# Kernel tuning notes

Measured on AMD Instinct MI355X. Metric: run time of the kernel, lower is better.

Reference implementation:

```python
import jax, jax.numpy as jnp
import numpy as np

OUTCOMES = [8, 8, 8, 8, 8, 8]           # concept outcome counts (concepts_order)
N_TOTAL = int(np.prod(OUTCOMES))        # 262144 joint states
N_VALID = 8192                          # admissible states
B, D = 4096, 1024


def setup_inputs() -> dict:
    key = jax.random.key(0)
    k1, k2 = jax.random.split(key)
    embeddings = jax.random.normal(k1, (B, D), dtype=jnp.float32)
    W = jax.random.normal(k2, (N_VALID, D), dtype=jnp.float32) * 0.02
    b = jnp.zeros((N_VALID,), dtype=jnp.float32)
    # unique sorted admissible-state indices, like torch.argwhere(mask)
    rng = np.random.default_rng(0)
    valid_states = jnp.asarray(
        np.sort(rng.choice(N_TOTAL, size=N_VALID, replace=False)).astype(np.int32))
    return {"embeddings": embeddings, "W": W, "b": b, "valid_states": valid_states}


def reference(embeddings, W, b, valid_states):
    # softmax over valid states: [B, N_VALID]
    probs = jax.nn.softmax(embeddings @ W.T + b, axis=1)
    probs_t = probs.T  # [N_VALID, B] for leading-axis segment reduction
    marginals = []
    stride = N_TOTAL
    for n_i in OUTCOMES:
        stride //= n_i
        # digit of each valid joint-state index along this concept's axis
        digit = (valid_states // stride) % n_i  # [N_VALID]
        # equivalent to scattering probs into the full joint tensor and
        # summing over all other concept axes, without materializing it
        m = jax.ops.segment_sum(probs_t, digit, num_segments=n_i).T  # [B, n_i]
        marginals.append(m)
    return jnp.stack(marginals)  # [n_concepts, B, 8]
```

## Files before the change

kernel.cpp:

```cpp
#include <hip/hip_runtime.h>
#include <hip/hip_bf16.h>
#include <cstdint>
#include <cstddef>

typedef __bf16 bf16_t;
typedef bf16_t bf16x8 __attribute__((ext_vector_type(8)));
typedef bf16_t bf16x4 __attribute__((ext_vector_type(4)));
typedef float  f32x4  __attribute__((ext_vector_type(4)));
typedef unsigned int u32;

#define BROWS 4096
#define NV    8192
#define KD    1024
#define NT    16
#define ST    48
#define LOG2E 1.44269504088896340736f

#define GLL(gsrc, ldst) \
  __builtin_amdgcn_global_load_lds((const __attribute__((address_space(1))) u32*)(gsrc), \
                                   (__attribute__((address_space(3))) u32*)(ldst), 16, 0, 0)
#define FENCE asm volatile("" ::: "memory")

__global__ void prep_kernel(const float* __restrict__ E, const float* __restrict__ W,
                            const int* __restrict__ vs,
                            bf16_t* __restrict__ Eb, bf16_t* __restrict__ Wb,
                            bf16_t* __restrict__ s2t) {
  const int nE = BROWS * KD / 4;
  const int nW = NV * KD / 4;
  const int nS = ST * NV / 8;
  const int nT = nE + nW + nS;
  int idx = blockIdx.x * blockDim.x + threadIdx.x;
  int stride = gridDim.x * blockDim.x;
  for (int i = idx; i < nT; i += stride) {
    if (i < nE + nW) {
      const float4* s; bf16x4* d; int j;
      if (i < nE) { s = (const float4*)E; d = (bf16x4*)Eb; j = i; }
      else        { s = (const float4*)W; d = (bf16x4*)Wb; j = i - nE; }
      float4 v = s[j];
      bf16x4 o;
      o[0] = (bf16_t)v.x; o[1] = (bf16_t)v.y; o[2] = (bf16_t)v.z; o[3] = (bf16_t)v.w;
      d[j] = o;
    } else {
      int u  = i - nE - nW;
      int b  = u >> 10;
      int i0 = (u & 1023) * 8;
      int base = i0 ^ ((b & 7) << 3);
      int c = b >> 3, d = b & 7, sh = 15 - 3 * c;
      bf16x8 o;
#pragma unroll
      for (int e = 0; e < 8; ++e)
        o[e] = (bf16_t)((((vs[base + e] >> sh) & 7) == d) ? 1.0f : 0.0f);
      *(bf16x8*)(s2t + (size_t)b * NV + i0) = o;
    }
  }
}

__global__ __launch_bounds__(512, 2)
void gemm_fused_kernel(const bf16_t* __restrict__ W, const bf16_t* __restrict__ E,
                       const float* __restrict__ bias, const bf16_t* __restrict__ s2t,
                       float* __restrict__ part) {
  __shared__ __align__(16) char lds[2][65536];
  #define AKH0 0
  #define AKH1 16384
  #define BKH0 32768
  #define BKH1 49152

  const int t    = threadIdx.x;
  const int lane = t & 63;
  const int wv   = t >> 6;
  const int wm   = wv >> 2;
  const int wn   = wv & 3;
  const int fr   = lane & 15;
  const int fq   = lane >> 4;

  int bid = blockIdx.x;
  int wg  = (bid & 7) * 64 + (bid >> 3);
  const int stile = wg >> 4;
  const int btile = wg & 15;
  const int st0 = stile * 256;
  const int bt0 = btile * 256;

  const int srow = lane >> 2;
  const int skel = ((lane & 3) ^ ((lane >> 3) & 3)) * 8;
  const bf16_t* aptr = W + (size_t)(st0 + wv * 32 + srow) * KD + skel;
  const bf16_t* bptr = E + (size_t)(bt0 + wv * 32 + srow) * KD + skel;
  const int dchunk = (wv * 2) * 1024;

  const int xsw    = (fr & 6) << 3;
  const int a_base = wm * 8192 + ((fr * 64 + fq * 16) ^ xsw);
  const int b_base = wn * 4096 + ((fr * 64 + fq * 16) ^ xsw);

  f32x4 acc[8][4] = {};

  GLL(aptr,                &lds[0][AKH0 + dchunk]);
  GLL(aptr + 16 * KD,      &lds[0][AKH0 + dchunk + 1024]);
  GLL(bptr,                &lds[0][BKH0 + dchunk]);
  GLL(bptr + 16 * KD,      &lds[0][BKH0 + dchunk + 1024]);
  GLL(aptr + 32,           &lds[0][AKH1 + dchunk]);
  GLL(aptr + 32 + 16 * KD, &lds[0][AKH1 + dchunk + 1024]);
  GLL(bptr + 32,           &lds[0][BKH1 + dchunk]);
  GLL(bptr + 32 + 16 * KD, &lds[0][BKH1 + dchunk + 1024]);
  asm volatile("s_waitcnt vmcnt(0)" ::: "memory");
  __builtin_amdgcn_s_barrier();
  FENCE;

  int cur = 0;
  for (int kt = 0; kt < NT; ++kt) {
    const char* bufp = lds[cur];
    char* nbuf = lds[cur ^ 1];
    const bool pf = (kt + 1 < NT);

    bf16x8 a0[8], b0[4], a1[8], b1[4];

#pragma unroll
    for (int n = 0; n < 4; ++n)
      b0[n] = *(const bf16x8*)(bufp + b_base + BKH0 + n * 1024);
#pragma unroll
    for (int m = 0; m < 8; ++m)
      a0[m] = *(const bf16x8*)(bufp + a_base + AKH0 + m * 1024);

    if (pf) {
      const bf16_t* an = aptr + (kt + 1) * 64;
      const bf16_t* bn = bptr + (kt + 1) * 64;
      GLL(an,                &nbuf[AKH0 + dchunk]);
      GLL(an + 16 * KD,      &nbuf[AKH0 + dchunk + 1024]);
      GLL(bn,                &nbuf[BKH0 + dchunk]);
      GLL(bn + 16 * KD,      &nbuf[BKH0 + dchunk + 1024]);
      GLL(an + 32,           &nbuf[AKH1 + dchunk]);
      GLL(an + 32 + 16 * KD, &nbuf[AKH1 + dchunk + 1024]);
      GLL(bn + 32,           &nbuf[BKH1 + dchunk]);
      GLL(bn + 32 + 16 * KD, &nbuf[BKH1 + dchunk + 1024]);
    }

#pragma unroll
    for (int n = 0; n < 4; ++n)
      b1[n] = *(const bf16x8*)(bufp + b_base + BKH1 + n * 1024);
#pragma unroll
    for (int m = 0; m < 8; ++m)
      a1[m] = *(const bf16x8*)(bufp + a_base + AKH1 + m * 1024);

    __builtin_amdgcn_s_setprio(1);
#pragma unroll
    for (int m = 0; m < 8; ++m)
#pragma unroll
      for (int n = 0; n < 4; ++n)
        acc[m][n] = __builtin_amdgcn_mfma_f32_16x16x32_bf16(a0[m], b0[n], acc[m][n], 0, 0, 0);
#pragma unroll
    for (int m = 0; m < 8; ++m)
#pragma unroll
      for (int n = 0; n < 4; ++n)
        acc[m][n] = __builtin_amdgcn_mfma_f32_16x16x32_bf16(a1[m], b1[n], acc[m][n], 0, 0, 0);
    __builtin_amdgcn_s_setprio(0);

    asm volatile("s_waitcnt vmcnt(0)" ::: "memory");
    __builtin_amdgcn_sched_barrier(0);
    __builtin_amdgcn_s_barrier();
    FENCE;
    cur ^= 1;
  }

  char* const ldsf = &lds[0][0];
  {
#pragma unroll
    for (int q = 0; q < 3; ++q) {
      const bf16_t* src = s2t + (size_t)(wv * 6 + q * 2 + (lane >> 5)) * NV
                          + st0 + (lane & 31) * 8;
      GLL(src, ldsf + 65536 + wv * 3072 + q * 1024);
    }
  }

  float* const ppart = part + (size_t)bt0 * (32 * ST) + (size_t)stile * ST;

#pragma unroll
  for (int pass = 0; pass < 2; ++pass) {
    if ((wn >> 1) == pass) {
#pragma unroll
      for (int m = 0; m < 8; ++m) {
        const float4 bb = *(const float4*)&bias[st0 + wm * 128 + m * 16 + fq * 4];
#pragma unroll
        for (int n = 0; n < 4; ++n) {
          bf16x4 ev;
          ev[0] = (bf16_t)exp2f((acc[m][n][0] + bb.x) * LOG2E);
          ev[1] = (bf16_t)exp2f((acc[m][n][1] + bb.y) * LOG2E);
          ev[2] = (bf16_t)exp2f((acc[m][n][2] + bb.z) * LOG2E);
          ev[3] = (bf16_t)exp2f((acc[m][n][3] + bb.w) * LOG2E);
          const int jh = (wn & 1) * 64 + n * 16 + fr;
          const int ib = (wm * 128 + m * 16 + fq * 4) * 2;
          *(bf16x4*)(ldsf + jh * 512 + (ib ^ ((fr & 7) << 4))) = ev;
        }
      }
    }
    if (pass == 0) asm volatile("s_waitcnt vmcnt(0)" ::: "memory");
    __syncthreads();

    f32x4 acc2[3] = {{0.f,0.f,0.f,0.f},{0.f,0.f,0.f,0.f},{0.f,0.f,0.f,0.f}};
#pragma unroll
    for (int k2 = 0; k2 < 8; ++k2) {
      const int ko2 = (k2 * 64 + fq * 16) ^ ((fr & 7) << 4);
      const bf16x8 ea = *(const bf16x8*)(ldsf + (wv * 16 + fr) * 512 + ko2);
#pragma unroll
      for (int n2 = 0; n2 < 3; ++n2) {
        const bf16x8 sb = *(const bf16x8*)(ldsf + 65536 + (n2 * 16 + fr) * 512 + ko2);
        acc2[n2] = __builtin_amdgcn_mfma_f32_16x16x32_bf16(ea, sb, acc2[n2], 0, 0, 0);
      }
    }
    const int jg = pass * 128 + wv * 16 + fq * 4;
#pragma unroll
    for (int n2 = 0; n2 < 3; ++n2)
#pragma unroll
      for (int r = 0; r < 4; ++r)
        ppart[(size_t)(jg + r) * (32 * ST) + n2 * 16 + fr] = acc2[n2][r];
    __syncthreads();
  }
}

__global__ __launch_bounds__(64)
void reduce_kernel(const float* __restrict__ part, float* __restrict__ out) {
  const int b = blockIdx.x;
  const int t = threadIdx.x;
  __shared__ float fin[ST];
  if (t < ST) {
    const float* p = part + (size_t)b * (32 * ST) + t;
    float s = 0.f;
#pragma unroll
    for (int mt = 0; mt < 32; ++mt)
      s += p[mt * ST];
    fin[t] = s;
  }
  __syncthreads();
  if (t < ST) {
    float total = fin[0] + fin[1] + fin[2] + fin[3] + fin[4] + fin[5] + fin[6] + fin[7];
    out[(size_t)(t >> 3) * BROWS * 8 + (size_t)b * 8 + (t & 7)] = fin[t] / total;
  }
}

extern "C" void kernel_launch(void* const* d_in, const int* in_sizes, int n_in,
                              void* d_out, int out_size, void* d_ws, size_t ws_size,
                              hipStream_t stream) {
  const float* E    = (const float*)d_in[0];
  const float* W    = (const float*)d_in[1];
  const float* bias = (const float*)d_in[2];
  const int*   vs   = (const int*)d_in[3];
  float* out = (float*)d_out;

  char* ws = (char*)d_ws;
  size_t off = 0;
  bf16_t* Eb   = (bf16_t*)(ws + off); off += (size_t)BROWS * KD * 2;
  bf16_t* Wb   = (bf16_t*)(ws + off); off += (size_t)NV * KD * 2;
  bf16_t* s2t  = (bf16_t*)(ws + off); off += (size_t)ST * NV * 2;
  float*  part = (float*)(ws + off);  off += (size_t)BROWS * 32 * ST * 4;

  prep_kernel<<<3072, 256, 0, stream>>>(E, W, vs, Eb, Wb, s2t);
  gemm_fused_kernel<<<512, 512, 0, stream>>>(Wb, Eb, bias, s2t, part);
  reduce_kernel<<<BROWS, 64, 0, stream>>>(part, out);
}
```

Measured before the change: 99.30 us.

## Shrink GEMM tiles to 128x128 with 256 threads and more blocks per CU

Restructures the fused GEMM-softmax-segment kernel from 256x256 tiles with 512 threads to 128x128 tiles with 256 threads, a K step of 32 and a 45KB shared buffer. The goal is 3 blocks per CU and a 2048-block grid, for better occupancy and load balance across CUs. The s2t indicator matrix is now loaded at kernel start with a swizzle applied on load, so the prep kernel no longer pre-swizzles it. In exchange, per-tile operand reuse drops and the partial-sum buffer doubles, which adds traffic to the reduce kernel.

```diff
diff --git a/kernel.cpp b/kernel.cpp
--- a/kernel.cpp
+++ b/kernel.cpp
@@ -12,8 +12,9 @@
 #define BROWS 4096
 #define NV    8192
 #define KD    1024
-#define NT    16
+#define NT    32
 #define ST    48
+#define NST   64
 #define LOG2E 1.44269504088896340736f
 
 #define GLL(gsrc, ldst) \
@@ -44,112 +45,95 @@
       int u  = i - nE - nW;
       int b  = u >> 10;
       int i0 = (u & 1023) * 8;
-      int base = i0 ^ ((b & 7) << 3);
       int c = b >> 3, d = b & 7, sh = 15 - 3 * c;
       bf16x8 o;
 #pragma unroll
       for (int e = 0; e < 8; ++e)
-        o[e] = (bf16_t)((((vs[base + e] >> sh) & 7) == d) ? 1.0f : 0.0f);
+        o[e] = (bf16_t)((((vs[i0 + e] >> sh) & 7) == d) ? 1.0f : 0.0f);
       *(bf16x8*)(s2t + (size_t)b * NV + i0) = o;
     }
   }
 }
 
-__global__ __launch_bounds__(512, 2)
+__global__ __launch_bounds__(256, 3)
 void gemm_fused_kernel(const bf16_t* __restrict__ W, const bf16_t* __restrict__ E,
                        const float* __restrict__ bias, const bf16_t* __restrict__ s2t,
                        float* __restrict__ part) {
-  __shared__ __align__(16) char lds[2][65536];
-  #define AKH0 0
-  #define AKH1 16384
-  #define BKH0 32768
-  #define BKH1 49152
+  __shared__ __align__(16) char lds[45056];
 
   const int t    = threadIdx.x;
   const int lane = t & 63;
   const int wv   = t >> 6;
-  const int wm   = wv >> 2;
-  const int wn   = wv & 3;
+  const int wm   = wv >> 1;
+  const int wn   = wv & 1;
   const int fr   = lane & 15;
   const int fq   = lane >> 4;
 
   int bid = blockIdx.x;
-  int wg  = (bid & 7) * 64 + (bid >> 3);
-  const int stile = wg >> 4;
-  const int btile = wg & 15;
-  const int st0 = stile * 256;
-  const int bt0 = btile * 256;
+  int wg  = (bid & 7) * 256 + (bid >> 3);
+  const int stile = wg >> 5;
+  const int btile = wg & 31;
+  const int st0 = stile * 128;
+  const int bt0 = btile * 128;
 
   const int srow = lane >> 2;
   const int skel = ((lane & 3) ^ ((lane >> 3) & 3)) * 8;
   const bf16_t* aptr = W + (size_t)(st0 + wv * 32 + srow) * KD + skel;
   const bf16_t* bptr = E + (size_t)(bt0 + wv * 32 + srow) * KD + skel;
-  const int dchunk = (wv * 2) * 1024;
+  const int dchunk = wv * 2048;
 
   const int xsw    = (fr & 6) << 3;
-  const int a_base = wm * 8192 + ((fr * 64 + fq * 16) ^ xsw);
-  const int b_base = wn * 4096 + ((fr * 64 + fq * 16) ^ xsw);
-
-  f32x4 acc[8][4] = {};
-
-  GLL(aptr,                &lds[0][AKH0 + dchunk]);
-  GLL(aptr + 16 * KD,      &lds[0][AKH0 + dchunk + 1024]);
-  GLL(bptr,                &lds[0][BKH0 + dchunk]);
-  GLL(bptr + 16 * KD,      &lds[0][BKH0 + dchunk + 1024]);
-  GLL(aptr + 32,           &lds[0][AKH1 + dchunk]);
-  GLL(aptr + 32 + 16 * KD, &lds[0][AKH1 + dchunk + 1024]);
-  GLL(bptr + 32,           &lds[0][BKH1 + dchunk]);
-  GLL(bptr + 32 + 16 * KD, &lds[0][BKH1 + dchunk + 1024]);
+  const int a_base = wm * 4096 + ((fr * 64 + fq * 16) ^ xsw);
+  const int b_base = 8192 + wn * 4096 + ((fr * 64 + fq * 16) ^ xsw);
+
+  f32x4 acc[4][4] = {};
+
+  GLL(aptr,           &lds[0 + dchunk]);
+  GLL(aptr + 16 * KD, &lds[0 + dchunk + 1024]);
+  GLL(bptr,           &lds[8192 + dchunk]);
+  GLL(bptr + 16 * KD, &lds[8192 + dchunk + 1024]);
+  {
+#pragma unroll
+    for (int q = 0; q < 3; ++q) {
+      const int c = wv * 3 + q;
+      const int r = c * 4 + (lane >> 4);
+      const bf16_t* src = s2t + (size_t)r * NV + st0 + (((lane & 15) * 8) ^ ((r & 7) << 3));
+      GLL(src, &lds[32768 + c * 1024]);
+    }
+  }
   asm volatile("s_waitcnt vmcnt(0)" ::: "memory");
   __builtin_amdgcn_s_barrier();
   FENCE;
 
   int cur = 0;
   for (int kt = 0; kt < NT; ++kt) {
-    const char* bufp = lds[cur];
-    char* nbuf = lds[cur ^ 1];
+    const char* bufp = &lds[cur * 16384];
+    char* nbuf = &lds[(cur ^ 1) * 16384];
     const bool pf = (kt + 1 < NT);
 
-    bf16x8 a0[8], b0[4], a1[8], b1[4];
-
+    bf16x8 a[4], b[4];
 #pragma unroll
     for (int n = 0; n < 4; ++n)
-      b0[n] = *(const bf16x8*)(bufp + b_base + BKH0 + n * 1024);
-#pragma unroll
-    for (int m = 0; m < 8; ++m)
-      a0[m] = *(const bf16x8*)(bufp + a_base + AKH0 + m * 1024);
+      b[n] = *(const bf16x8*)(bufp + b_base + n * 1024);
+#pragma unroll
+    for (int m = 0; m < 4; ++m)
+      a[m] = *(const bf16x8*)(bufp + a_base + m * 1024);
 
     if (pf) {
-      const bf16_t* an = aptr + (kt + 1) * 64;
-      const bf16_t* bn = bptr + (kt + 1) * 64;
-      GLL(an,                &nbuf[AKH0 + dchunk]);
-      GLL(an + 16 * KD,      &nbuf[AKH0 + dchunk + 1024]);
-      GLL(bn,                &nbuf[BKH0 + dchunk]);
-      GLL(bn + 16 * KD,      &nbuf[BKH0 + dchunk + 1024]);
-      GLL(an + 32,           &nbuf[AKH1 + dchunk]);
-      GLL(an + 32 + 16 * KD, &nbuf[AKH1 + dchunk + 1024]);
-      GLL(bn + 32,           &nbuf[BKH1 + dchunk]);
-      GLL(bn + 32 + 16 * KD, &nbuf[BKH1 + dchunk + 1024]);
-    }
-
-#pragma unroll
-    for (int n = 0; n < 4; ++n)
-      b1[n] = *(const bf16x8*)(bufp + b_base + BKH1 + n * 1024);
-#pragma unroll
-    for (int m = 0; m < 8; ++m)
-      a1[m] = *(const bf16x8*)(bufp + a_base + AKH1 + m * 1024);
+      const bf16_t* an = aptr + (kt + 1) * 32;
+      const bf16_t* bn = bptr + (kt + 1) * 32;
+      GLL(an,           nbuf + 0 + dchunk);
+      GLL(an + 16 * KD, nbuf + 0 + dchunk + 1024);
+      GLL(bn,           nbuf + 8192 + dchunk);
+      GLL(bn + 16 * KD, nbuf + 8192 + dchunk + 1024);
+    }
 
     __builtin_amdgcn_s_setprio(1);
 #pragma unroll
-    for (int m = 0; m < 8; ++m)
+    for (int m = 0; m < 4; ++m)
 #pragma unroll
       for (int n = 0; n < 4; ++n)
-        acc[m][n] = __builtin_amdgcn_mfma_f32_16x16x32_bf16(a0[m], b0[n], acc[m][n], 0, 0, 0);
-#pragma unroll
-    for (int m = 0; m < 8; ++m)
-#pragma unroll
-      for (int n = 0; n < 4; ++n)
-        acc[m][n] = __builtin_amdgcn_mfma_f32_16x16x32_bf16(a1[m], b1[n], acc[m][n], 0, 0, 0);
+        acc[m][n] = __builtin_amdgcn_mfma_f32_16x16x32_bf16(a[m], b[n], acc[m][n], 0, 0, 0);
     __builtin_amdgcn_s_setprio(0);
 
     asm volatile("s_waitcnt vmcnt(0)" ::: "memory");
@@ -159,58 +143,45 @@
     cur ^= 1;
   }
 
-  char* const ldsf = &lds[0][0];
-  {
-#pragma unroll
-    for (int q = 0; q < 3; ++q) {
-      const bf16_t* src = s2t + (size_t)(wv * 6 + q * 2 + (lane >> 5)) * NV
-                          + st0 + (lane & 31) * 8;
-      GLL(src, ldsf + 65536 + wv * 3072 + q * 1024);
-    }
-  }
-
-  float* const ppart = part + (size_t)bt0 * (32 * ST) + (size_t)stile * ST;
-
-#pragma unroll
-  for (int pass = 0; pass < 2; ++pass) {
-    if ((wn >> 1) == pass) {
-#pragma unroll
-      for (int m = 0; m < 8; ++m) {
-        const float4 bb = *(const float4*)&bias[st0 + wm * 128 + m * 16 + fq * 4];
-#pragma unroll
-        for (int n = 0; n < 4; ++n) {
-          bf16x4 ev;
-          ev[0] = (bf16_t)exp2f((acc[m][n][0] + bb.x) * LOG2E);
-          ev[1] = (bf16_t)exp2f((acc[m][n][1] + bb.y) * LOG2E);
-          ev[2] = (bf16_t)exp2f((acc[m][n][2] + bb.z) * LOG2E);
-          ev[3] = (bf16_t)exp2f((acc[m][n][3] + bb.w) * LOG2E);
-          const int jh = (wn & 1) * 64 + n * 16 + fr;
-          const int ib = (wm * 128 + m * 16 + fq * 4) * 2;
-          *(bf16x4*)(ldsf + jh * 512 + (ib ^ ((fr & 7) << 4))) = ev;
-        }
+#pragma unroll
+  for (int m = 0; m < 4; ++m) {
+    const float4 bb = *(const float4*)&bias[st0 + wm * 64 + m * 16 + fq * 4];
+#pragma unroll
+    for (int n = 0; n < 4; ++n) {
+      bf16x4 ev;
+      ev[0] = (bf16_t)exp2f((acc[m][n][0] + bb.x) * LOG2E);
+      ev[1] = (bf16_t)exp2f((acc[m][n][1] + bb.y) * LOG2E);
+      ev[2] = (bf16_t)exp2f((acc[m][n][2] + bb.z) * LOG2E);
+      ev[3] = (bf16_t)exp2f((acc[m][n][3] + bb.w) * LOG2E);
+      const int jh = wn * 64 + n * 16 + fr;
+      const int ib = wm * 128 + m * 32 + fq * 8;
+      *(bf16x4*)(&lds[jh * 256 + (ib ^ ((fr & 7) << 4))]) = ev;
+    }
+  }
+  __syncthreads();
+
+  float* const ppart = part + (size_t)bt0 * (NST * ST) + (size_t)stile * ST;
+  f32x4 acc2[2][3] = {};
+#pragma unroll
+  for (int g = 0; g < 2; ++g)
+#pragma unroll
+    for (int k2 = 0; k2 < 4; ++k2) {
+      const int ko2 = (k2 * 64 + fq * 16) ^ ((fr & 7) << 4);
+      const bf16x8 ea = *(const bf16x8*)(&lds[(wv * 32 + g * 16 + fr) * 256 + ko2]);
+#pragma unroll
+      for (int n2 = 0; n2 < 3; ++n2) {
+        const bf16x8 sb = *(const bf16x8*)(&lds[32768 + (n2 * 16 + fr) * 256 + ko2]);
+        acc2[g][n2] = __builtin_amdgcn_mfma_f32_16x16x32_bf16(ea, sb, acc2[g][n2], 0, 0, 0);
       }
     }
-    if (pass == 0) asm volatile("s_waitcnt vmcnt(0)" ::: "memory");
-    __syncthreads();
-
-    f32x4 acc2[3] = {{0.f,0.f,0.f,0.f},{0.f,0.f,0.f,0.f},{0.f,0.f,0.f,0.f}};
-#pragma unroll
-    for (int k2 = 0; k2 < 8; ++k2) {
-      const int ko2 = (k2 * 64 + fq * 16) ^ ((fr & 7) << 4);
-      const bf16x8 ea = *(const bf16x8*)(ldsf + (wv * 16 + fr) * 512 + ko2);
-#pragma unroll
-      for (int n2 = 0; n2 < 3; ++n2) {
-        const bf16x8 sb = *(const bf16x8*)(ldsf + 65536 + (n2 * 16 + fr) * 512 + ko2);
-        acc2[n2] = __builtin_amdgcn_mfma_f32_16x16x32_bf16(ea, sb, acc2[n2], 0, 0, 0);
-      }
-    }
-    const int jg = pass * 128 + wv * 16 + fq * 4;
+#pragma unroll
+  for (int g = 0; g < 2; ++g) {
+    const int jg = wv * 32 + g * 16 + fq * 4;
 #pragma unroll
     for (int n2 = 0; n2 < 3; ++n2)
 #pragma unroll
       for (int r = 0; r < 4; ++r)
-        ppart[(size_t)(jg + r) * (32 * ST) + n2 * 16 + fr] = acc2[n2][r];
-    __syncthreads();
+        ppart[(size_t)(jg + r) * (NST * ST) + n2 * 16 + fr] = acc2[g][n2][r];
   }
 }
 
@@ -220,10 +191,10 @@
   const int t = threadIdx.x;
   __shared__ float fin[ST];
   if (t < ST) {
-    const float* p = part + (size_t)b * (32 * ST) + t;
+    const float* p = part + (size_t)b * (NST * ST) + t;
     float s = 0.f;
 #pragma unroll
-    for (int mt = 0; mt < 32; ++mt)
+    for (int mt = 0; mt < NST; ++mt)
       s += p[mt * ST];
     fin[t] = s;
   }
@@ -248,9 +219,9 @@
   bf16_t* Eb   = (bf16_t*)(ws + off); off += (size_t)BROWS * KD * 2;
   bf16_t* Wb   = (bf16_t*)(ws + off); off += (size_t)NV * KD * 2;
   bf16_t* s2t  = (bf16_t*)(ws + off); off += (size_t)ST * NV * 2;
-  float*  part = (float*)(ws + off);  off += (size_t)BROWS * 32 * ST * 4;
+  float*  part = (float*)(ws + off);  off += (size_t)BROWS * NST * ST * 4;
 
   prep_kernel<<<3072, 256, 0, stream>>>(E, W, vs, Eb, Wb, s2t);
-  gemm_fused_kernel<<<512, 512, 0, stream>>>(Wb, Eb, bias, s2t, part);
+  gemm_fused_kernel<<<2048, 256, 0, stream>>>(Wb, Eb, bias, s2t, part);
   reduce_kernel<<<BROWS, 64, 0, stream>>>(part, out);
 }
```

New measurement: 108.8 us. +9.6%, slower.
